# Kernel tuning notes

Measured on AMD Instinct MI355X. Metric: run time of the kernel, lower is better.

The kernel has to match this reference:

```python
import jax, jax.numpy as jnp
import numpy as np

NLAYERS, NHEAD, ATTN_LEN, DMODEL, DHID, NTOKEN = 9, 2, 5, 128, 512, 2
HD = DMODEL // NHEAD
B, T, F = 4, 4096, 128
INV_SQRT_HD = 1.0 / float(np.sqrt(HD))


def setup_inputs() -> dict:
    key = jax.random.key(0)
    ks = iter(jax.random.split(key, 64))
    def w(shape, s=0.02):
        return jax.random.normal(next(ks), shape, jnp.float32) * s
    return dict(
        x=jax.random.normal(next(ks), (B, T, F), jnp.float32),
        conv1_w=w((32, 1, 5, 3)), conv1_b=jnp.zeros((32,), jnp.float32),
        conv2_w=w((64, 32, 1, 12)), conv2_b=jnp.zeros((64,), jnp.float32),
        conv3_w=w((DMODEL, 64, 3, 6)), conv3_b=jnp.zeros((DMODEL,), jnp.float32),
        ln1_s=jnp.ones((NLAYERS, DMODEL), jnp.float32), ln1_b=jnp.zeros((NLAYERS, DMODEL), jnp.float32),
        ln2_s=jnp.ones((NLAYERS, DMODEL), jnp.float32), ln2_b=jnp.zeros((NLAYERS, DMODEL), jnp.float32),
        Wq=w((NLAYERS, DMODEL, DMODEL)), bq=jnp.zeros((NLAYERS, DMODEL), jnp.float32),
        Wk=w((NLAYERS, DMODEL, DMODEL)), bk=jnp.zeros((NLAYERS, DMODEL), jnp.float32),
        Wv=w((NLAYERS, DMODEL, DMODEL)), bv=jnp.zeros((NLAYERS, DMODEL), jnp.float32),
        Wo=w((NLAYERS, DMODEL, DMODEL)), bo=jnp.zeros((NLAYERS, DMODEL), jnp.float32),
        Er=w((NLAYERS, NHEAD, ATTN_LEN, HD)),
        W1=w((NLAYERS, DMODEL, DHID)), b1=jnp.zeros((NLAYERS, DHID), jnp.float32),
        W2=w((NLAYERS, DHID, DMODEL)), b2=jnp.zeros((NLAYERS, DMODEL), jnp.float32),
        Wout=w((DMODEL, NTOKEN)), bout=jnp.zeros((NTOKEN,), jnp.float32),
        Wt=w((DMODEL, 300)), bt=jnp.zeros((300,), jnp.float32),
    )


def _ln(x, s, b, eps=1e-5):
    m = x.mean(-1, keepdims=True)
    v = ((x - m) ** 2).mean(-1, keepdims=True)
    return (x - m) * jax.lax.rsqrt(v + eps) * s + b


def _conv(x, w, b, pad_h):
    y = jax.lax.conv_general_dilated(x, w, (1, 1), ((pad_h, pad_h), (0, 0)),
                                     dimension_numbers=('NCHW', 'OIHW', 'NCHW'))
    return y + b[None, :, None, None]


def _pool3(x):
    # MaxPool2d(kernel=(1,3), stride=(1,3)) on freq axis
    return jax.lax.reduce_window(x, -jnp.inf, jax.lax.max, (1, 1, 1, 3), (1, 1, 1, 3), 'VALID')


def _attn(x, Wq, bq, Wk, bk, Wv, bv, Wo, bo, Er, layer):
    # Dilated windowed attention: query t attends to t + (k - attn_len//2)*2^layer
    Bb, Tt, D = x.shape
    dil = 2 ** layer
    c = ATTN_LEN // 2
    q = (x @ Wq + bq).reshape(Bb, Tt, NHEAD, HD)
    k = (x @ Wk + bk).reshape(Bb, Tt, NHEAD, HD)
    v = (x @ Wv + bv).reshape(Bb, Tt, NHEAD, HD)
    offs = (jnp.arange(Tt)[:, None] + (jnp.arange(ATTN_LEN) - c)[None, :] * dil)  # (T, a)
    valid = (offs >= 0) & (offs < Tt)
    idx = jnp.clip(offs, 0, Tt - 1)
    kg = k[:, idx]  # (B, T, a, H, hd)
    vg = v[:, idx]
    scores = (jnp.einsum('bthd,btahd->bhta', q, kg)
              + jnp.einsum('bthd,had->bhta', q, Er)) * INV_SQRT_HD
    scores = jnp.where(valid[None, None], scores, -jnp.inf)
    a = jax.nn.softmax(scores, axis=-1)
    out = jnp.einsum('bhta,btahd->bthd', a, vg).reshape(Bb, Tt, D)
    return out @ Wo + bo


def _forward(x, conv1_w, conv1_b, conv2_w, conv2_b, conv3_w, conv3_b,
             ln1_s, ln1_b, ln2_s, ln2_b, Wq, bq, Wk, bk, Wv, bv, Wo, bo, Er,
             W1, b1, W2, b2, Wout, bout, Wt, bt):
    h = x[:, None]                                    # (B,1,T,F)
    h = jax.nn.relu(_pool3(_conv(h, conv1_w, conv1_b, 2)))
    h = jax.nn.relu(_pool3(_conv(h, conv2_w, conv2_b, 0)))
    h = jax.nn.relu(_pool3(_conv(h, conv3_w, conv3_b, 1)))  # (B,D,T,1)
    h = h[:, :, :, 0].transpose(0, 2, 1)              # (B,T,D)
    skips = []
    for l in range(NLAYERS):
        skip = _attn(_ln(h, ln1_s[l], ln1_b[l]), Wq[l], bq[l], Wk[l], bk[l],
                     Wv[l], bv[l], Wo[l], bo[l], Er[l], l)
        h = h + skip
        z = _ln(h, ln2_s[l], ln2_b[l])
        h = h + jax.nn.relu(z @ W1[l] + b1[l]) @ W2[l] + b2[l]
        skips.append(skip)
    out = jax.nn.relu(h) @ Wout + bout                # (B,T,ntoken)
    t = jax.nn.relu(sum(skips)).mean(axis=1) @ Wt + bt  # (B,300)
    return out, t


def reference(x, conv1_w, conv1_b, conv2_w, conv2_b, conv3_w, conv3_b,
              ln1_s, ln1_b, ln2_s, ln2_b, Wq, bq, Wk, bk, Wv, bv, Wo, bo, Er,
              W1, b1, W2, b2, Wout, bout, Wt, bt):
    return _forward(x, conv1_w, conv1_b, conv2_w, conv2_b, conv3_w, conv3_b,
                    ln1_s, ln1_b, ln2_s, ln2_b, Wq, bq, Wk, bk, Wv, bv, Wo, bo, Er,
                    W1, b1, W2, b2, Wout, bout, Wt, bt)
```

## Files before the change

kernel.cpp:

```cpp
#include <hip/hip_runtime.h>

#define T_ 4096
#define B_ 4

typedef unsigned short u16;
typedef __bf16 bf16x8 __attribute__((ext_vector_type(8)));
typedef float f32x4 __attribute__((ext_vector_type(4)));

__device__ inline void splitbf(float v, u16& h, u16& l) {
  __bf16 hb = (__bf16)v;
  float r = v - (float)hb;
  __bf16 lb = (__bf16)r;
  h = __builtin_bit_cast(u16, hb);
  l = __builtin_bit_cast(u16, lb);
}

#define MFMA(a,b,c) __builtin_amdgcn_mfma_f32_16x16x32_bf16((a),(b),(c),0,0,0)

__global__ __launch_bounds__(256) void k_conv12m(
    const float* __restrict__ x, const float* __restrict__ w1,
    const float* __restrict__ b1,
    const u16* __restrict__ wh, const u16* __restrict__ wl,
    const float* __restrict__ b2,
    u16* __restrict__ oh, u16* __restrict__ ol)
{
  __shared__ float sx[12][130];
  __shared__ float w1s[480];
  __shared__ float b1s[32];
  __shared__ u16 sh[8*43*40];
  __shared__ u16 sl[8*43*40];
  __shared__ float dmp[4][15][66];
  const int tid = threadIdx.x;
  const int t0 = blockIdx.x * 8;
  const int b = blockIdx.y;
  const float* xb = x + (size_t)b*T_*128;
  for (int i = tid; i < 1536; i += 256) {
    int r = i >> 7, c = i & 127;
    int t = t0 - 2 + r;
    sx[r][c] = (t >= 0 && t < T_) ? xb[t*128 + c] : 0.f;
  }
  for (int i = tid; i < 480; i += 256) w1s[i] = w1[i];
  if (tid < 32) b1s[tid] = b1[tid];
  for (int i = tid; i < 320; i += 256) {
    int tt = i / 40, c = i - tt*40;
    sh[(tt*43 + 42)*40 + c] = 0;
    sl[(tt*43 + 42)*40 + c] = 0;
  }
  __syncthreads();
  for (int i = tid; i < 10752; i += 256) {
    int c1 = i & 31;
    int wp = (i >> 5) % 42;
    int tt = i / 1344;
    float m = -1e30f;
    #pragma unroll
    for (int j = 0; j < 3; j++) {
      float acc = 0.f;
      int wb = wp*3 + j;
      #pragma unroll
      for (int kh = 0; kh < 5; kh++)
        #pragma unroll
        for (int kw = 0; kw < 3; kw++)
          acc += sx[tt+kh][wb+kw] * w1s[c1*15 + kh*3 + kw];
      m = fmaxf(m, acc);
    }
    float v = fmaxf(m + b1s[c1], 0.f);
    u16 hh, ll; splitbf(v, hh, ll);
    int dd = (tt*43 + wp)*40 + c1;
    sh[dd] = hh; sl[dd] = ll;
  }
  __syncthreads();
  const int lane = tid & 63;
  const int wid = tid >> 6;
  const int lr = lane & 15;
  const int lk8 = (lane >> 4) * 8;
  f32x4 acc[2][2][4] = {};
  #pragma unroll 3
  for (int kw = 0; kw < 12; kw++) {
    bf16x8 bh[4], bl[4];
    #pragma unroll
    for (int nf = 0; nf < 4; nf++) {
      int go = ((nf*12 + kw) << 9) + (lane << 3);
      bh[nf] = *(const bf16x8*)(wh + go);
      bl[nf] = *(const bf16x8*)(wl + go);
    }
    #pragma unroll
    for (int tp = 0; tp < 2; tp++) {
      int tloc = wid*2 + tp;
      #pragma unroll
      for (int mf = 0; mf < 2; mf++) {
        int lofs = (tloc*43 + mf*16 + lr + kw)*40 + lk8;
        bf16x8 ah = *(const bf16x8*)&sh[lofs];
        bf16x8 al = *(const bf16x8*)&sl[lofs];
        #pragma unroll
        for (int nf = 0; nf < 4; nf++) {
          acc[tp][mf][nf] = MFMA(ah, bl[nf], acc[tp][mf][nf]);
          acc[tp][mf][nf] = MFMA(al, bh[nf], acc[tp][mf][nf]);
          acc[tp][mf][nf] = MFMA(ah, bh[nf], acc[tp][mf][nf]);
        }
      }
    }
  }
  const int lg = lane >> 4;
  for (int tp = 0; tp < 2; tp++) {
    int t = t0 + wid*2 + tp;
    for (int half = 0; half < 2; half++) {
      #pragma unroll
      for (int mf = 0; mf < 2; mf++)
        #pragma unroll
        for (int r = 0; r < 4; r++) {
          int grow = mf*16 + lg*4 + r;
          int lrow = grow - half*15;
          if (lrow >= 0 && lrow < 15) {
            #pragma unroll
            for (int nf = 0; nf < 4; nf++)
              dmp[wid][lrow][nf*16 + lr] = acc[tp][mf][nf][r];
          }
        }
      asm volatile("s_waitcnt lgkmcnt(0)" ::: "memory");
      #pragma unroll
      for (int it = 0; it < 5; it++) {
        float v = fmaxf(fmaxf(dmp[wid][it*3][lane], dmp[wid][it*3+1][lane]),
                        dmp[wid][it*3+2][lane]);
        v = fmaxf(v + b2[lane], 0.f);
        u16 hh, ll; splitbf(v, hh, ll);
        size_t o = (size_t)((b*T_ + t)*10 + half*5 + it)*64 + lane;
        oh[o] = hh; ol[o] = ll;
      }
      asm volatile("s_waitcnt lgkmcnt(0)" ::: "memory");
    }
  }
}

__global__ __launch_bounds__(256) void k_conv3m(
    const u16* __restrict__ ih, const u16* __restrict__ il,
    const u16* __restrict__ wh, const u16* __restrict__ wl,
    const float* __restrict__ b3, float* __restrict__ hout)
{
  __shared__ u16 sh[18*720];
  __shared__ u16 sl[18*720];
  __shared__ float dmp[48][132];
  const int tid = threadIdx.x;
  const int t0 = (blockIdx.x & 255) * 16;
  const int b = blockIdx.y;
  for (int i = tid; i < 1440; i += 256) {
    int cg = i & 7;
    int w = (i >> 3) % 10;
    int tt = i / 80;
    int t = t0 - 1 + tt;
    int dd = tt*720 + w*72 + cg*8;
    if (t >= 0 && t < T_) {
      size_t so = (size_t)((b*T_ + t)*10 + w)*64 + cg*8;
      *(ulonglong2*)&sh[dd] = *(const ulonglong2*)&ih[so];
      *(ulonglong2*)&sl[dd] = *(const ulonglong2*)&il[so];
    } else {
      ulonglong2 z; z.x = 0; z.y = 0;
      *(ulonglong2*)&sh[dd] = z;
      *(ulonglong2*)&sl[dd] = z;
    }
  }
  __syncthreads();
  const int lane = tid & 63;
  const int wid = tid >> 6;
  const int lr = lane & 15;
  const int lk8 = (lane >> 4) * 8;
  int tlm[3], wom[3];
  #pragma unroll
  for (int mf = 0; mf < 3; mf++) {
    int r = mf*16 + lr;
    tlm[mf] = r / 3;
    wom[mf] = r - tlm[mf]*3;
  }
  f32x4 acc[3][2] = {};
  #pragma unroll 2
  for (int kh = 0; kh < 3; kh++) {
    #pragma unroll
    for (int kw = 0; kw < 6; kw++) {
      #pragma unroll
      for (int chh = 0; chh < 2; chh++) {
        int s = (kh*6 + kw)*2 + chh;
        int ch = chh*32;
        bf16x8 bh[2], bl[2];
        #pragma unroll
        for (int nfl = 0; nfl < 2; nfl++) {
          int go = (((wid*2 + nfl)*36 + s) << 9) + (lane << 3);
          bh[nfl] = *(const bf16x8*)(wh + go);
          bl[nfl] = *(const bf16x8*)(wl + go);
        }
        #pragma unroll
        for (int mf = 0; mf < 3; mf++) {
          int lofs = (tlm[mf] + kh)*720 + (wom[mf] + kw)*72 + ch + lk8;
          bf16x8 ah = *(const bf16x8*)&sh[lofs];
          bf16x8 al = *(const bf16x8*)&sl[lofs];
          #pragma unroll
          for (int nfl = 0; nfl < 2; nfl++) {
            acc[mf][nfl] = MFMA(ah, bl[nfl], acc[mf][nfl]);
            acc[mf][nfl] = MFMA(al, bh[nfl], acc[mf][nfl]);
            acc[mf][nfl] = MFMA(ah, bh[nfl], acc[mf][nfl]);
          }
        }
      }
    }
  }
  const int lg = lane >> 4;
  #pragma unroll
  for (int mf = 0; mf < 3; mf++)
    #pragma unroll
    for (int r = 0; r < 4; r++) {
      int row = mf*16 + lg*4 + r;
      #pragma unroll
      for (int nfl = 0; nfl < 2; nfl++)
        dmp[row][wid*32 + nfl*16 + lr] = acc[mf][nfl][r];
    }
  __syncthreads();
  for (int i = tid; i < 2048; i += 256) {
    int c3 = i & 127;
    int tt = i >> 7;
    float v = fmaxf(fmaxf(dmp[tt*3][c3], dmp[tt*3+1][c3]), dmp[tt*3+2][c3]);
    v = fmaxf(v + b3[c3], 0.f);
    hout[(size_t)(b*T_ + t0 + tt)*128 + c3] = v;
  }
}

__device__ inline float wave_sum(float v) {
  #pragma unroll
  for (int m = 1; m < 64; m <<= 1) v += __shfl_xor(v, m, 64);
  return v;
}

__global__ __launch_bounds__(256) void k_ln(
    const float* __restrict__ in, const float* __restrict__ sc,
    const float* __restrict__ bi, u16* __restrict__ oh, u16* __restrict__ ol)
{
  const int lane = threadIdx.x & 63;
  const int row = blockIdx.x*4 + (threadIdx.x >> 6);
  float a = in[row*128 + lane];
  float c = in[row*128 + 64 + lane];
  float mean = wave_sum(a + c) * (1.f/128.f);
  float d0 = a - mean, d1 = c - mean;
  float var = wave_sum(d0*d0 + d1*d1) * (1.f/128.f);
  float rs = rsqrtf(var + 1e-5f);
  float v0 = d0*rs*sc[lane]    + bi[lane];
  float v1 = d1*rs*sc[64+lane] + bi[64+lane];
  u16 h0, l0, h1, l1;
  splitbf(v0, h0, l0); splitbf(v1, h1, l1);
  oh[row*128 + lane] = h0;      ol[row*128 + lane] = l0;
  oh[row*128 + 64 + lane] = h1; ol[row*128 + 64 + lane] = l1;
}

__device__ inline void prep_fr(const float* __restrict__ src,
                               u16* __restrict__ dh, u16* __restrict__ dl,
                               int K, int N, int matStride, int idx)
{
  int mat = idx / (K*N);
  int rem = idx - mat*(K*N);
  int k = rem / N;
  int n = rem - k*N;
  float v = src[idx];
  u16 h, l; splitbf(v, h, l);
  int nt = n >> 4, ks = k >> 5, ksub = k & 31;
  size_t o = (size_t)mat*matStride + (size_t)((nt*(K>>5) + ks) << 9)
           + (((ksub >> 3) << 4) + (n & 15))*8 + (ksub & 7);
  dh[o] = h; dl[o] = l;
}

__global__ __launch_bounds__(256) void k_wprep_all(
    const float* __restrict__ Wq, const float* __restrict__ Wk,
    const float* __restrict__ Wv, const float* __restrict__ Wo,
    const float* __restrict__ W1, const float* __restrict__ W2,
    const float* __restrict__ c2w, const float* __restrict__ c3w,
    u16* wqkv_h, u16* wqkv_l, u16* wo_h, u16* wo_l,
    u16* w1t_h, u16* w1t_l, u16* w2t_h, u16* w2t_l,
    u16* wc2_h, u16* wc2_l, u16* wc3_h, u16* wc3_l)
{
  const int bid = blockIdx.x;
  const int tid = threadIdx.x;
  if (bid < 576) {
    prep_fr(Wq, wqkv_h, wqkv_l, 128, 128, 49152, bid*256 + tid);
  } else if (bid < 1152) {
    prep_fr(Wk, wqkv_h + 16384, wqkv_l + 16384, 128, 128, 49152, (bid-576)*256 + tid);
  } else if (bid < 1728) {
    prep_fr(Wv, wqkv_h + 32768, wqkv_l + 32768, 128, 128, 49152, (bid-1152)*256 + tid);
  } else if (bid < 2304) {
    prep_fr(Wo, wo_h, wo_l, 128, 128, 16384, (bid-1728)*256 + tid);
  } else if (bid < 4608) {
    prep_fr(W1, w1t_h, w1t_l, 128, 512, 65536, (bid-2304)*256 + tid);
  } else if (bid < 6912) {
    prep_fr(W2, w2t_h, w2t_l, 512, 128, 65536, (bid-4608)*256 + tid);
  } else if (bid < 7008) {
    int idx = (bid-6912)*256 + tid;
    int c2 = idx / 384;
    int rem = idx - c2*384;
    int c1 = rem / 12;
    int kw = rem - c1*12;
    float v = c2w[idx];
    u16 h, l; splitbf(v, h, l);
    size_t o = (size_t)((((c2 >> 4)*12 + kw) << 9))
             + (((c1 >> 3) << 4) + (c2 & 15))*8 + (c1 & 7);
    wc2_h[o] = h; wc2_l[o] = l;
  } else {
    int idx = (bid-7008)*256 + tid;
    int c3 = idx / 1152;
    int rem = idx - c3*1152;
    int c2 = rem / 18;
    int khkw = rem - c2*18;
    float v = c3w[idx];
    u16 h, l; splitbf(v, h, l);
    int s = khkw*2 + (c2 >> 5);
    int c = c2 & 31;
    size_t o = (size_t)((((c3 >> 4)*36 + s) << 9))
             + (((c >> 3) << 4) + (c3 & 15))*8 + (c & 7);
    wc3_h[o] = h; wc3_l[o] = l;
  }
}

__global__ __launch_bounds__(256) void k_gqkv(
    const u16* __restrict__ Ah, const u16* __restrict__ Al,
    const u16* __restrict__ Wh, const u16* __restrict__ Wl,
    const float* __restrict__ bq, const float* __restrict__ bk,
    const float* __restrict__ bv, float* __restrict__ outbase)
{
  __shared__ u16 sAh[16*136], sAl[16*136];
  const int tid = threadIdx.x;
  const int m0 = blockIdx.x * 16;
  const int z = blockIdx.y;
  const u16* wh = Wh + z*16384;
  const u16* wl = Wl + z*16384;
  const float* bias = (z == 0) ? bq : (z == 1) ? bk : bv;
  float* C = outbase + (size_t)z*2097152;
  {
    int row = tid >> 4, c8 = tid & 15;
    *(ulonglong2*)&sAh[row*136 + c8*8] = *(const ulonglong2*)&Ah[(size_t)(m0+row)*128 + c8*8];
    *(ulonglong2*)&sAl[row*136 + c8*8] = *(const ulonglong2*)&Al[(size_t)(m0+row)*128 + c8*8];
  }
  __syncthreads();
  const int lane = tid & 63, nq = tid >> 6;
  const int lr = lane & 15, lg = lane >> 4, l8 = lg*8;
  f32x4 acc[2] = {};
  #pragma unroll
  for (int ks = 0; ks < 4; ks++) {
    bf16x8 ah = *(const bf16x8*)&sAh[lr*136 + ks*32 + l8];
    bf16x8 al = *(const bf16x8*)&sAl[lr*136 + ks*32 + l8];
    #pragma unroll
    for (int nf = 0; nf < 2; nf++) {
      int go = (((nq*2 + nf)*4 + ks) << 9) + (lane << 3);
      bf16x8 bh = *(const bf16x8*)(wh + go);
      bf16x8 bl = *(const bf16x8*)(wl + go);
      acc[nf] = MFMA(ah, bl, acc[nf]);
      acc[nf] = MFMA(al, bh, acc[nf]);
      acc[nf] = MFMA(ah, bh, acc[nf]);
    }
  }
  #pragma unroll
  for (int nf = 0; nf < 2; nf++) {
    int col = nq*32 + nf*16 + lr;
    float bb = bias[col];
    #pragma unroll
    for (int r = 0; r < 4; r++)
      C[(size_t)(m0 + lg*4 + r)*128 + col] = acc[nf][r] + bb;
  }
}

__global__ __launch_bounds__(256) void k_attnwo(
    const float* __restrict__ qb, const float* __restrict__ kb,
    const float* __restrict__ vb, const float* __restrict__ Er,
    const u16* __restrict__ Wh, const u16* __restrict__ Wl,
    const float* __restrict__ bo, const float* __restrict__ sc,
    const float* __restrict__ bi,
    float* __restrict__ hbuf, float* __restrict__ ssum, int skip_init,
    u16* __restrict__ oh, u16* __restrict__ ol, int dil)
{
  __shared__ u16 sAh[16*136], sAl[16*136];
  __shared__ float dmp[16*132];
  const int tid = threadIdx.x, lane = tid & 63, wv = tid >> 6;
  const int m0 = blockIdx.x * 16;
  const int b = m0 >> 12;
  const int t0 = m0 & 4095;
  for (int rr = 0; rr < 4; rr++) {
    int r = wv*4 + rr;
    int t = t0 + r;
    int bt = m0 + r;
    #pragma unroll
    for (int h = 0; h < 2; h++) {
      float qd = qb[(size_t)bt*128 + h*64 + lane];
      float s[5];
      int tpc_arr[5];
      #pragma unroll
      for (int a = 0; a < 5; a++) {
        int tp = t + (a-2)*dil;
        bool valid = (tp >= 0 && tp < T_);
        int tpc = tp < 0 ? 0 : (tp > T_-1 ? T_-1 : tp);
        tpc_arr[a] = tpc;
        float kd = kb[(size_t)(b*T_ + tpc)*128 + h*64 + lane];
        float er = Er[(h*5 + a)*64 + lane];
        float p = qd * (kd + er);
        p = wave_sum(p);
        s[a] = valid ? p * 0.125f : -1e30f;
      }
      float mx = s[0];
      #pragma unroll
      for (int a = 1; a < 5; a++) mx = fmaxf(mx, s[a]);
      float p[5], psum = 0.f;
      #pragma unroll
      for (int a = 0; a < 5; a++) { p[a] = __expf(s[a]-mx); psum += p[a]; }
      float inv = 1.f/psum;
      float o = 0.f;
      #pragma unroll
      for (int a = 0; a < 5; a++)
        o += p[a] * vb[(size_t)(b*T_ + tpc_arr[a])*128 + h*64 + lane];
      float vo = o * inv;
      u16 hh, ll; splitbf(vo, hh, ll);
      sAh[r*136 + h*64 + lane] = hh;
      sAl[r*136 + h*64 + lane] = ll;
    }
  }
  __syncthreads();
  const int lr = lane & 15, lg = lane >> 4, l8 = lg*8;
  const int nq = wv;
  f32x4 acc[2] = {};
  #pragma unroll
  for (int ks = 0; ks < 4; ks++) {
    bf16x8 ah = *(const bf16x8*)&sAh[lr*136 + ks*32 + l8];
    bf16x8 al = *(const bf16x8*)&sAl[lr*136 + ks*32 + l8];
    #pragma unroll
    for (int nf = 0; nf < 2; nf++) {
      int go = (((nq*2 + nf)*4 + ks) << 9) + (lane << 3);
      bf16x8 bh = *(const bf16x8*)(Wh + go);
      bf16x8 bl = *(const bf16x8*)(Wl + go);
      acc[nf] = MFMA(ah, bl, acc[nf]);
      acc[nf] = MFMA(al, bh, acc[nf]);
      acc[nf] = MFMA(ah, bh, acc[nf]);
    }
  }
  #pragma unroll
  for (int nf = 0; nf < 2; nf++) {
    int col = nq*32 + nf*16 + lr;
    float bb = bo[col];
    #pragma unroll
    for (int r = 0; r < 4; r++) {
      int row = lg*4 + r;
      size_t o = (size_t)(m0 + row)*128 + col;
      float val = acc[nf][r] + bb;
      if (skip_init) ssum[o] = val; else ssum[o] += val;
      float hn = hbuf[o] + val;
      hbuf[o] = hn;
      dmp[row*132 + col] = hn;
    }
  }
  __syncthreads();
  const int row = tid >> 4, p = tid & 15;
  float xv[8], s = 0.f;
  const float* dp = &dmp[row*132 + p*8];
  #pragma unroll
  for (int i = 0; i < 8; i++) { xv[i] = dp[i]; s += xv[i]; }
  s += __shfl_xor(s, 1); s += __shfl_xor(s, 2);
  s += __shfl_xor(s, 4); s += __shfl_xor(s, 8);
  float mean = s * (1.f/128.f);
  float v = 0.f;
  #pragma unroll
  for (int i = 0; i < 8; i++) { float d = xv[i]-mean; v += d*d; }
  v += __shfl_xor(v, 1); v += __shfl_xor(v, 2);
  v += __shfl_xor(v, 4); v += __shfl_xor(v, 8);
  float rs = rsqrtf(v*(1.f/128.f) + 1e-5f);
  size_t gro = (size_t)(m0 + row)*128;
  #pragma unroll
  for (int i = 0; i < 8; i++) {
    int c = p*8 + i;
    float y = (xv[i]-mean)*rs*sc[c] + bi[c];
    u16 hh, ll; splitbf(y, hh, ll);
    oh[gro + c] = hh; ol[gro + c] = ll;
  }
}

__global__ __launch_bounds__(256) void k_ffn(
    const u16* __restrict__ Ah, const u16* __restrict__ Al,
    const u16* __restrict__ W1h, const u16* __restrict__ W1l,
    const float* __restrict__ b1,
    const u16* __restrict__ W2h, const u16* __restrict__ W2l,
    const float* __restrict__ b2,
    const float* __restrict__ sc, const float* __restrict__ bi, int do_ln,
    float* __restrict__ hbuf, u16* __restrict__ oh, u16* __restrict__ ol)
{
  __shared__ u16 sAh[16*136], sAl[16*136];
  __shared__ u16 hidH[2][16*136], hidL[2][16*136];
  __shared__ float dmp[16*132];
  const int tid = threadIdx.x;
  const int m0 = blockIdx.x * 16;
  {
    int row = tid >> 4, c8 = tid & 15;
    *(ulonglong2*)&sAh[row*136 + c8*8] = *(const ulonglong2*)&Ah[(size_t)(m0+row)*128 + c8*8];
    *(ulonglong2*)&sAl[row*136 + c8*8] = *(const ulonglong2*)&Al[(size_t)(m0+row)*128 + c8*8];
  }
  __syncthreads();
  const int lane = tid & 63, nq = tid >> 6;
  const int lr = lane & 15, lg = lane >> 4, l8 = lg*8;
  f32x4 acc2[2] = {};
  for (int c = 0; c < 4; c++) {
    f32x4 acc1[2] = {};
    #pragma unroll
    for (int ks = 0; ks < 4; ks++) {
      bf16x8 ah = *(const bf16x8*)&sAh[lr*136 + ks*32 + l8];
      bf16x8 al = *(const bf16x8*)&sAl[lr*136 + ks*32 + l8];
      #pragma unroll
      for (int nf = 0; nf < 2; nf++) {
        int go = (((c*8 + nq*2 + nf)*4 + ks) << 9) + (lane << 3);
        bf16x8 bh = *(const bf16x8*)(W1h + go);
        bf16x8 bl = *(const bf16x8*)(W1l + go);
        acc1[nf] = MFMA(ah, bl, acc1[nf]);
        acc1[nf] = MFMA(al, bh, acc1[nf]);
        acc1[nf] = MFMA(ah, bh, acc1[nf]);
      }
    }
    __syncthreads();
    #pragma unroll
    for (int nf = 0; nf < 2; nf++) {
      int col = nq*32 + nf*16 + lr;
      float bb = b1[c*128 + col];
      #pragma unroll
      for (int r = 0; r < 4; r++) {
        int row = lg*4 + r;
        float hv = fmaxf(acc1[nf][r] + bb, 0.f);
        u16 hh, ll; splitbf(hv, hh, ll);
        hidH[c & 1][row*136 + col] = hh;
        hidL[c & 1][row*136 + col] = ll;
      }
    }
    __syncthreads();
    #pragma unroll
    for (int ks = 0; ks < 4; ks++) {
      bf16x8 ah = *(const bf16x8*)&hidH[c & 1][lr*136 + ks*32 + l8];
      bf16x8 al = *(const bf16x8*)&hidL[c & 1][lr*136 + ks*32 + l8];
      #pragma unroll
      for (int nf = 0; nf < 2; nf++) {
        int go = (((nq*2 + nf)*16 + c*4 + ks) << 9) + (lane << 3);
        bf16x8 bh = *(const bf16x8*)(W2h + go);
        bf16x8 bl = *(const bf16x8*)(W2l + go);
        acc2[nf] = MFMA(ah, bl, acc2[nf]);
        acc2[nf] = MFMA(al, bh, acc2[nf]);
        acc2[nf] = MFMA(ah, bh, acc2[nf]);
      }
    }
  }
  #pragma unroll
  for (int nf = 0; nf < 2; nf++) {
    int col = nq*32 + nf*16 + lr;
    float bb = b2[col];
    #pragma unroll
    for (int r = 0; r < 4; r++) {
      int row = lg*4 + r;
      size_t o = (size_t)(m0 + row)*128 + col;
      float hn = hbuf[o] + acc2[nf][r] + bb;
      hbuf[o] = hn;
      dmp[row*132 + col] = hn;
    }
  }
  if (!do_ln) return;
  __syncthreads();
  const int row = tid >> 4, p = tid & 15;
  float xv[8], s = 0.f;
  const float* dp = &dmp[row*132 + p*8];
  #pragma unroll
  for (int i = 0; i < 8; i++) { xv[i] = dp[i]; s += xv[i]; }
  s += __shfl_xor(s, 1); s += __shfl_xor(s, 2);
  s += __shfl_xor(s, 4); s += __shfl_xor(s, 8);
  float mean = s * (1.f/128.f);
  float v = 0.f;
  #pragma unroll
  for (int i = 0; i < 8; i++) { float d = xv[i]-mean; v += d*d; }
  v += __shfl_xor(v, 1); v += __shfl_xor(v, 2);
  v += __shfl_xor(v, 4); v += __shfl_xor(v, 8);
  float rs = rsqrtf(v*(1.f/128.f) + 1e-5f);
  size_t gro = (size_t)(m0 + row)*128;
  #pragma unroll
  for (int i = 0; i < 8; i++) {
    int c2 = p*8 + i;
    float y = (xv[i]-mean)*rs*sc[c2] + bi[c2];
    u16 hh, ll; splitbf(y, hh, ll);
    oh[gro + c2] = hh; ol[gro + c2] = ll;
  }
}

__global__ __launch_bounds__(256) void k_out(
    const float* __restrict__ h, const float* __restrict__ Wout,
    const float* __restrict__ bout, float* __restrict__ out)
{
  int idx = blockIdx.x*256 + threadIdx.x;
  int bt = idx >> 1, j = idx & 1;
  float acc = bout[j];
  const float* hp = &h[bt*128];
  #pragma unroll 4
  for (int k2 = 0; k2 < 128; k2++)
    acc += fmaxf(hp[k2], 0.f) * Wout[k2*2 + j];
  out[idx] = acc;
}

__global__ __launch_bounds__(256) void k_red1(
    const float* __restrict__ ss, float* __restrict__ part)
{
  __shared__ float red[256];
  int b = blockIdx.x >> 5, g = blockIdx.x & 31;
  int c = threadIdx.x & 127, hf = threadIdx.x >> 7;
  float acc = 0.f;
  for (int i2 = 0; i2 < 64; i2++) {
    int t = g*128 + i2*2 + hf;
    acc += fmaxf(ss[(b*T_ + t)*128 + c], 0.f);
  }
  red[threadIdx.x] = acc;
  __syncthreads();
  if (threadIdx.x < 128)
    part[(b*32+g)*128 + threadIdx.x] = red[threadIdx.x] + red[threadIdx.x+128];
}

__global__ __launch_bounds__(512) void k_tail2(
    const float* __restrict__ part, const float* __restrict__ Wt,
    const float* __restrict__ btb, float* __restrict__ out)
{
  __shared__ float mb[512];
  const int tid = threadIdx.x;
  int b = tid >> 7, c = tid & 127;
  float s = 0.f;
  for (int g = 0; g < 32; g++) s += part[(b*32+g)*128 + c];
  mb[tid] = s * (1.f/4096.f);
  __syncthreads();
  for (int i = tid; i < 1200; i += 512) {
    int bb = i / 300, j = i - bb*300;
    float acc = btb[j];
    #pragma unroll 4
    for (int k2 = 0; k2 < 128; k2++)
      acc += mb[bb*128 + k2] * Wt[k2*300 + j];
    out[32768 + i] = acc;
  }
}

extern "C" void kernel_launch(void* const* d_in, const int* in_sizes, int n_in,
                              void* d_out, int out_size, void* d_ws, size_t ws_size,
                              hipStream_t stream)
{
  const float* x    = (const float*)d_in[0];
  const float* c1w  = (const float*)d_in[1];
  const float* c1b  = (const float*)d_in[2];
  const float* c2w  = (const float*)d_in[3];
  const float* c2b  = (const float*)d_in[4];
  const float* c3w  = (const float*)d_in[5];
  const float* c3b  = (const float*)d_in[6];
  const float* ln1s = (const float*)d_in[7];
  const float* ln1b = (const float*)d_in[8];
  const float* ln2s = (const float*)d_in[9];
  const float* ln2b = (const float*)d_in[10];
  const float* Wq   = (const float*)d_in[11];
  const float* bq   = (const float*)d_in[12];
  const float* Wk   = (const float*)d_in[13];
  const float* bk   = (const float*)d_in[14];
  const float* Wv   = (const float*)d_in[15];
  const float* bv   = (const float*)d_in[16];
  const float* Wo   = (const float*)d_in[17];
  const float* bo   = (const float*)d_in[18];
  const float* Er   = (const float*)d_in[19];
  const float* W1   = (const float*)d_in[20];
  const float* b1   = (const float*)d_in[21];
  const float* W2   = (const float*)d_in[22];
  const float* b2   = (const float*)d_in[23];
  const float* Wout = (const float*)d_in[24];
  const float* bout = (const float*)d_in[25];
  const float* Wt   = (const float*)d_in[26];
  const float* bt   = (const float*)d_in[27];

  char* W = (char*)d_ws;
  u16* c2o_h = (u16*)W;
  u16* c2o_l = (u16*)(W + 20971520);
  char* RB = W + 33554432;
  float* qb  = (float*)RB;
  float* kb  = qb + 2097152;
  float* vb2 = qb + 4194304;
  u16* xh    = (u16*)(RB + 25165824);
  u16* xlo   = (u16*)(RB + 29360128);
  char* RC = W + 67108864;
  float* hbuf = (float*)RC;
  float* ssum = (float*)(RC + 8388608);
  u16* wqkv_h = (u16*)(RC + 16777216);
  u16* wqkv_l = wqkv_h + 442368;
  u16* wo_h   = wqkv_l + 442368;
  u16* wo_l   = wo_h + 147456;
  u16* w1t_h  = wo_l + 147456;
  u16* w1t_l  = w1t_h + 589824;
  u16* w2t_h  = w1t_l + 589824;
  u16* w2t_l  = w2t_h + 589824;
  u16* wc2_h  = w2t_l + 589824;
  u16* wc2_l  = wc2_h + 24576;
  u16* wc3_h  = wc2_l + 24576;
  u16* wc3_l  = wc3_h + 147456;
  float* part  = (float*)(wc3_l + 147456);
  float* meanb = part + 16384;
  float* outf  = (float*)d_out;
  (void)meanb;

  k_wprep_all<<<7584, 256, 0, stream>>>(
      Wq, Wk, Wv, Wo, W1, W2, c2w, c3w,
      wqkv_h, wqkv_l, wo_h, wo_l, w1t_h, w1t_l, w2t_h, w2t_l,
      wc2_h, wc2_l, wc3_h, wc3_l);

  k_conv12m<<<dim3(512, B_), 256, 0, stream>>>(x, c1w, c1b, wc2_h, wc2_l, c2b,
                                               c2o_h, c2o_l);
  k_conv3m<<<dim3(256, B_), 256, 0, stream>>>(c2o_h, c2o_l, wc3_h, wc3_l, c3b, hbuf);

  k_ln<<<4096, 256, 0, stream>>>(hbuf, ln1s, ln1b, xh, xlo);

  for (int l = 0; l < 9; l++) {
    k_gqkv<<<dim3(1024, 3), 256, 0, stream>>>(
        xh, xlo, wqkv_h + l*49152, wqkv_l + l*49152,
        bq + l*128, bk + l*128, bv + l*128, qb);
    k_attnwo<<<1024, 256, 0, stream>>>(
        qb, kb, vb2, Er + l*640,
        wo_h + l*16384, wo_l + l*16384, bo + l*128,
        ln2s + l*128, ln2b + l*128,
        hbuf, ssum, (l == 0) ? 1 : 0, xh, xlo, 1 << l);
    k_ffn<<<1024, 256, 0, stream>>>(
        xh, xlo, w1t_h + l*65536, w1t_l + l*65536, b1 + l*512,
        w2t_h + l*65536, w2t_l + l*65536, b2 + l*128,
        ln1s + (l+1 < 9 ? (l+1)*128 : 0), ln1b + (l+1 < 9 ? (l+1)*128 : 0),
        (l < 8) ? 1 : 0,
        hbuf, xh, xlo);
  }

  k_out<<<128, 256, 0, stream>>>(hbuf, Wout, bout, outf);
  k_red1<<<128, 256, 0, stream>>>(ssum, part);
  k_tail2<<<1, 512, 0, stream>>>(part, Wt, bt, outf);
}
```

Baseline: 763.8 us.

## Fuse next-layer QKV projection into FFN kernel and widen row tiles

```diff
diff --git a/kernel.cpp b/kernel.cpp
--- a/kernel.cpp
+++ b/kernel.cpp
@@ -360,7 +360,7 @@
   }
 }
 
-__global__ __launch_bounds__(256) void k_attnwo(
+__global__ __launch_bounds__(512) void k_attnwo(
     const float* __restrict__ qb, const float* __restrict__ kb,
     const float* __restrict__ vb, const float* __restrict__ Er,
     const u16* __restrict__ Wh, const u16* __restrict__ Wl,
@@ -369,10 +369,10 @@
     float* __restrict__ hbuf, float* __restrict__ ssum, int skip_init,
     u16* __restrict__ oh, u16* __restrict__ ol, int dil)
 {
-  __shared__ u16 sAh[16*136], sAl[16*136];
-  __shared__ float dmp[16*132];
+  __shared__ u16 sAh[32*136], sAl[32*136];
+  __shared__ float dmp[32*132];
   const int tid = threadIdx.x, lane = tid & 63, wv = tid >> 6;
-  const int m0 = blockIdx.x * 16;
+  const int m0 = blockIdx.x * 32;
   const int b = m0 >> 12;
   const int t0 = m0 & 4095;
   for (int rr = 0; rr < 4; rr++) {
@@ -415,12 +415,12 @@
   }
   __syncthreads();
   const int lr = lane & 15, lg = lane >> 4, l8 = lg*8;
-  const int nq = wv;
+  const int mq = wv >> 2, nq = wv & 3;
   f32x4 acc[2] = {};
   #pragma unroll
   for (int ks = 0; ks < 4; ks++) {
-    bf16x8 ah = *(const bf16x8*)&sAh[lr*136 + ks*32 + l8];
-    bf16x8 al = *(const bf16x8*)&sAl[lr*136 + ks*32 + l8];
+    bf16x8 ah = *(const bf16x8*)&sAh[(mq*16 + lr)*136 + ks*32 + l8];
+    bf16x8 al = *(const bf16x8*)&sAl[(mq*16 + lr)*136 + ks*32 + l8];
     #pragma unroll
     for (int nf = 0; nf < 2; nf++) {
       int go = (((nq*2 + nf)*4 + ks) << 9) + (lane << 3);
@@ -437,7 +437,7 @@
     float bb = bo[col];
     #pragma unroll
     for (int r = 0; r < 4; r++) {
-      int row = lg*4 + r;
+      int row = mq*16 + lg*4 + r;
       size_t o = (size_t)(m0 + row)*128 + col;
       float val = acc[nf][r] + bb;
       if (skip_init) ssum[o] = val; else ssum[o] += val;
@@ -471,35 +471,38 @@
   }
 }
 
-__global__ __launch_bounds__(256) void k_ffn(
+__global__ __launch_bounds__(512) void k_ffnqkv(
     const u16* __restrict__ Ah, const u16* __restrict__ Al,
     const u16* __restrict__ W1h, const u16* __restrict__ W1l,
     const float* __restrict__ b1,
     const u16* __restrict__ W2h, const u16* __restrict__ W2l,
     const float* __restrict__ b2,
-    const float* __restrict__ sc, const float* __restrict__ bi, int do_ln,
-    float* __restrict__ hbuf, u16* __restrict__ oh, u16* __restrict__ ol)
-{
-  __shared__ u16 sAh[16*136], sAl[16*136];
-  __shared__ u16 hidH[2][16*136], hidL[2][16*136];
-  __shared__ float dmp[16*132];
-  const int tid = threadIdx.x;
-  const int m0 = blockIdx.x * 16;
+    float* __restrict__ hbuf, int do_qkv,
+    const float* __restrict__ sc, const float* __restrict__ bi,
+    const u16* __restrict__ Qh, const u16* __restrict__ Ql,
+    const float* __restrict__ bq, const float* __restrict__ bk,
+    const float* __restrict__ bv, float* __restrict__ qkvout)
+{
+  __shared__ u16 sAh[32*136], sAl[32*136];
+  __shared__ u16 hidH[2][32*136], hidL[2][32*136];
+  __shared__ float dmp[32*132];
+  const int tid = threadIdx.x, lane = tid & 63;
+  const int m0 = blockIdx.x * 32;
   {
     int row = tid >> 4, c8 = tid & 15;
     *(ulonglong2*)&sAh[row*136 + c8*8] = *(const ulonglong2*)&Ah[(size_t)(m0+row)*128 + c8*8];
     *(ulonglong2*)&sAl[row*136 + c8*8] = *(const ulonglong2*)&Al[(size_t)(m0+row)*128 + c8*8];
   }
   __syncthreads();
-  const int lane = tid & 63, nq = tid >> 6;
+  const int wv = tid >> 6, mq = wv >> 2, nq = wv & 3;
   const int lr = lane & 15, lg = lane >> 4, l8 = lg*8;
   f32x4 acc2[2] = {};
   for (int c = 0; c < 4; c++) {
     f32x4 acc1[2] = {};
     #pragma unroll
     for (int ks = 0; ks < 4; ks++) {
-      bf16x8 ah = *(const bf16x8*)&sAh[lr*136 + ks*32 + l8];
-      bf16x8 al = *(const bf16x8*)&sAl[lr*136 + ks*32 + l8];
+      bf16x8 ah = *(const bf16x8*)&sAh[(mq*16 + lr)*136 + ks*32 + l8];
+      bf16x8 al = *(const bf16x8*)&sAl[(mq*16 + lr)*136 + ks*32 + l8];
       #pragma unroll
       for (int nf = 0; nf < 2; nf++) {
         int go = (((c*8 + nq*2 + nf)*4 + ks) << 9) + (lane << 3);
@@ -517,7 +520,7 @@
       float bb = b1[c*128 + col];
       #pragma unroll
       for (int r = 0; r < 4; r++) {
-        int row = lg*4 + r;
+        int row = mq*16 + lg*4 + r;
         float hv = fmaxf(acc1[nf][r] + bb, 0.f);
         u16 hh, ll; splitbf(hv, hh, ll);
         hidH[c & 1][row*136 + col] = hh;
@@ -527,8 +530,8 @@
     __syncthreads();
     #pragma unroll
     for (int ks = 0; ks < 4; ks++) {
-      bf16x8 ah = *(const bf16x8*)&hidH[c & 1][lr*136 + ks*32 + l8];
-      bf16x8 al = *(const bf16x8*)&hidL[c & 1][lr*136 + ks*32 + l8];
+      bf16x8 ah = *(const bf16x8*)&hidH[c & 1][(mq*16 + lr)*136 + ks*32 + l8];
+      bf16x8 al = *(const bf16x8*)&hidL[c & 1][(mq*16 + lr)*136 + ks*32 + l8];
       #pragma unroll
       for (int nf = 0; nf < 2; nf++) {
         int go = (((nq*2 + nf)*16 + c*4 + ks) << 9) + (lane << 3);
@@ -546,36 +549,67 @@
     float bb = b2[col];
     #pragma unroll
     for (int r = 0; r < 4; r++) {
-      int row = lg*4 + r;
+      int row = mq*16 + lg*4 + r;
       size_t o = (size_t)(m0 + row)*128 + col;
       float hn = hbuf[o] + acc2[nf][r] + bb;
       hbuf[o] = hn;
       dmp[row*132 + col] = hn;
     }
   }
-  if (!do_ln) return;
-  __syncthreads();
-  const int row = tid >> 4, p = tid & 15;
-  float xv[8], s = 0.f;
-  const float* dp = &dmp[row*132 + p*8];
-  #pragma unroll
-  for (int i = 0; i < 8; i++) { xv[i] = dp[i]; s += xv[i]; }
-  s += __shfl_xor(s, 1); s += __shfl_xor(s, 2);
-  s += __shfl_xor(s, 4); s += __shfl_xor(s, 8);
-  float mean = s * (1.f/128.f);
-  float v = 0.f;
-  #pragma unroll
-  for (int i = 0; i < 8; i++) { float d = xv[i]-mean; v += d*d; }
-  v += __shfl_xor(v, 1); v += __shfl_xor(v, 2);
-  v += __shfl_xor(v, 4); v += __shfl_xor(v, 8);
-  float rs = rsqrtf(v*(1.f/128.f) + 1e-5f);
-  size_t gro = (size_t)(m0 + row)*128;
-  #pragma unroll
-  for (int i = 0; i < 8; i++) {
-    int c2 = p*8 + i;
-    float y = (xv[i]-mean)*rs*sc[c2] + bi[c2];
-    u16 hh, ll; splitbf(y, hh, ll);
-    oh[gro + c2] = hh; ol[gro + c2] = ll;
+  if (!do_qkv) return;
+  __syncthreads();
+  {
+    const int row = tid >> 4, p = tid & 15;
+    float xv[8], s = 0.f;
+    const float* dp = &dmp[row*132 + p*8];
+    #pragma unroll
+    for (int i = 0; i < 8; i++) { xv[i] = dp[i]; s += xv[i]; }
+    s += __shfl_xor(s, 1); s += __shfl_xor(s, 2);
+    s += __shfl_xor(s, 4); s += __shfl_xor(s, 8);
+    float mean = s * (1.f/128.f);
+    float v = 0.f;
+    #pragma unroll
+    for (int i = 0; i < 8; i++) { float d = xv[i]-mean; v += d*d; }
+    v += __shfl_xor(v, 1); v += __shfl_xor(v, 2);
+    v += __shfl_xor(v, 4); v += __shfl_xor(v, 8);
+    float rs = rsqrtf(v*(1.f/128.f) + 1e-5f);
+    #pragma unroll
+    for (int i = 0; i < 8; i++) {
+      int cc = p*8 + i;
+      float y = (xv[i]-mean)*rs*sc[cc] + bi[cc];
+      u16 hh, ll; splitbf(y, hh, ll);
+      sAh[row*136 + cc] = hh; sAl[row*136 + cc] = ll;
+    }
+  }
+  __syncthreads();
+  for (int z = 0; z < 3; z++) {
+    const u16* wh = Qh + z*16384;
+    const u16* wl = Ql + z*16384;
+    const float* bias = (z == 0) ? bq : (z == 1) ? bk : bv;
+    float* C = qkvout + (size_t)z*2097152;
+    f32x4 acc[2] = {};
+    #pragma unroll
+    for (int ks = 0; ks < 4; ks++) {
+      bf16x8 ah = *(const bf16x8*)&sAh[(mq*16 + lr)*136 + ks*32 + l8];
+      bf16x8 al = *(const bf16x8*)&sAl[(mq*16 + lr)*136 + ks*32 + l8];
+      #pragma unroll
+      for (int nf = 0; nf < 2; nf++) {
+        int go = (((nq*2 + nf)*4 + ks) << 9) + (lane << 3);
+        bf16x8 bh = *(const bf16x8*)(wh + go);
+        bf16x8 bl = *(const bf16x8*)(wl + go);
+        acc[nf] = MFMA(ah, bl, acc[nf]);
+        acc[nf] = MFMA(al, bh, acc[nf]);
+        acc[nf] = MFMA(ah, bh, acc[nf]);
+      }
+    }
+    #pragma unroll
+    for (int nf = 0; nf < 2; nf++) {
+      int col = nq*32 + nf*16 + lr;
+      float bb = bias[col];
+      #pragma unroll
+      for (int r = 0; r < 4; r++)
+        C[(size_t)(m0 + mq*16 + lg*4 + r)*128 + col] = acc[nf][r] + bb;
+    }
   }
 }
 
@@ -689,9 +723,7 @@
   u16* wc3_h  = wc2_l + 24576;
   u16* wc3_l  = wc3_h + 147456;
   float* part  = (float*)(wc3_l + 147456);
-  float* meanb = part + 16384;
   float* outf  = (float*)d_out;
-  (void)meanb;
 
   k_wprep_all<<<7584, 256, 0, stream>>>(
       Wq, Wk, Wv, Wo, W1, W2, c2w, c3w,
@@ -703,22 +735,23 @@
   k_conv3m<<<dim3(256, B_), 256, 0, stream>>>(c2o_h, c2o_l, wc3_h, wc3_l, c3b, hbuf);
 
   k_ln<<<4096, 256, 0, stream>>>(hbuf, ln1s, ln1b, xh, xlo);
+  k_gqkv<<<dim3(1024, 3), 256, 0, stream>>>(
+      xh, xlo, wqkv_h, wqkv_l, bq, bk, bv, qb);
 
   for (int l = 0; l < 9; l++) {
-    k_gqkv<<<dim3(1024, 3), 256, 0, stream>>>(
-        xh, xlo, wqkv_h + l*49152, wqkv_l + l*49152,
-        bq + l*128, bk + l*128, bv + l*128, qb);
-    k_attnwo<<<1024, 256, 0, stream>>>(
+    int ln = (l < 8) ? (l + 1) : 0;
+    k_attnwo<<<512, 512, 0, stream>>>(
         qb, kb, vb2, Er + l*640,
         wo_h + l*16384, wo_l + l*16384, bo + l*128,
         ln2s + l*128, ln2b + l*128,
         hbuf, ssum, (l == 0) ? 1 : 0, xh, xlo, 1 << l);
-    k_ffn<<<1024, 256, 0, stream>>>(
+    k_ffnqkv<<<512, 512, 0, stream>>>(
         xh, xlo, w1t_h + l*65536, w1t_l + l*65536, b1 + l*512,
         w2t_h + l*65536, w2t_l + l*65536, b2 + l*128,
-        ln1s + (l+1 < 9 ? (l+1)*128 : 0), ln1b + (l+1 < 9 ? (l+1)*128 : 0),
-        (l < 8) ? 1 : 0,
-        hbuf, xh, xlo);
+        hbuf, (l < 8) ? 1 : 0,
+        ln1s + ln*128, ln1b + ln*128,
+        wqkv_h + ln*49152, wqkv_l + ln*49152,
+        bq + ln*128, bk + ln*128, bv + ln*128, qb);
   }
 
   k_out<<<128, 256, 0, stream>>>(hbuf, Wout, bout, outf);
```

Result: faster. 712.6 us (-6.7%).
